# Performance work log

Hardware: AMD Instinct MI355X
Metric: run time of the kernel (lower is better)

Reference implementation:

```python
import jax, jax.numpy as jnp
import numpy as np

NUM_TOPICS = 100
VOCAB = 8192
MC_N = 20
MD_N = 20
LAMBDA_D = 0.7
LAMBDA_A = 100.0
WARMUP_RATIO = 0.5
NUM_EPOCHS = 200


def setup_inputs() -> dict:
    key = jax.random.key(0)
    k1, k2 = jax.random.split(key)
    beta = jax.random.normal(k1, (NUM_TOPICS, VOCAB), dtype=jnp.float32)
    W = jax.random.uniform(k2, (VOCAB, VOCAB), dtype=jnp.float32)
    # fill_diagonal_(1) in __init__
    d = jnp.arange(VOCAB)
    W = W.at[d, d].set(1.0)
    return {"beta": beta, "coherence_weight": W, "epoch": 120}


def reference(beta, coherence_weight, epoch):
    K, V = beta.shape
    rows = jnp.arange(K)[:, None]

    # --- Mc: top-Mc_n mask -> additive -99999 on non-topk entries ---
    _, mc_idx = jax.lax.top_k(beta, MC_N)                      # [K, Mc_n]
    Mc = jnp.zeros_like(beta).at[rows, mc_idx].set(1.0)        # [K, V]
    Mc_add = (1.0 - Mc) * (-99999.0)

    # softmax over masked beta is detached in the original
    p = jax.lax.stop_gradient(jax.nn.softmax(beta + Mc_add, axis=1))
    M = p @ coherence_weight                                    # [K, V]

    # row-wise min-max normalize, then Wc = 1 - normalized
    m_min = jnp.min(M, axis=1, keepdims=True)
    m_max = jnp.max(M, axis=1, keepdims=True)
    Wc = 1.0 - (M - m_min) / (m_max - m_min)

    loss = 100.0 * jax.nn.softmax(beta, axis=1) ** 2 * Wc       # [K, V]

    # --- diversity mask Md (lambda_d > 0.5 branch) ---
    _, md_idx = jax.lax.top_k(beta, MD_N)
    Md_mask = jnp.zeros_like(beta).at[rows, md_idx].set(1.0)    # [K, V]
    # Md[t, v] = any other row has v in its top-Md_n
    col_sum = jnp.sum(Md_mask, axis=0)                          # [V]
    Md = (col_sum[None, :] - Md_mask) > 0                       # [K, V] bool

    pos = jnp.sum(jnp.where(Md, loss, 0.0))
    neg = jnp.sum(jnp.where(Md, 0.0, loss))
    total = (pos * LAMBDA_D + neg * (1.0 - LAMBDA_D)) * 2.0

    warmup_epochs = int(WARMUP_RATIO * NUM_EPOCHS)              # 100
    lambda_a_delta = LAMBDA_A / warmup_epochs
    lambda_a = epoch * lambda_a_delta if epoch < warmup_epochs else LAMBDA_A
    return lambda_a * total
```

## Files before the change

kernel.cpp:

```cpp
#include <hip/hip_runtime.h>
#include <math.h>

#define NT 100
#define VOCAB 8192
#define TOPN 20
#define CHUNKS 8
#define CCOLS (VOCAB / CHUNKS)
#define CAP 4096

__global__ __launch_bounds__(256) void topk_kernel(
    const float* __restrict__ beta,
    int*   __restrict__ top_idx,
    float* __restrict__ top_p,
    float* __restrict__ rowstats)
{
    const int k = blockIdx.x;
    const int t = threadIdx.x;

    __shared__ float sred[4];
    __shared__ int   sredi[4];
    __shared__ float s_T;
    __shared__ int   s_base;
    __shared__ float cu[CAP];
    __shared__ unsigned short ci[CAP];
    __shared__ float s_winv[TOPN];
    __shared__ int   s_wini[TOPN];
    __shared__ float s_ps;

    const float* row = beta + (size_t)k * VOCAB;

    float4 r[8];
    float mx = -INFINITY;
#pragma unroll
    for (int i = 0; i < 8; ++i) {
        r[i] = *reinterpret_cast<const float4*>(row + (size_t)(i * 256 + t) * 4);
        mx = fmaxf(mx, fmaxf(fmaxf(r[i].x, r[i].y), fmaxf(r[i].z, r[i].w)));
    }
#pragma unroll
    for (int off = 32; off >= 1; off >>= 1) mx = fmaxf(mx, __shfl_down(mx, off));
    if ((t & 63) == 0) sred[t >> 6] = mx;
    __syncthreads();
    const float rowmax = fmaxf(fmaxf(sred[0], sred[1]), fmaxf(sred[2], sred[3]));

    float T = rowmax - 2.0f;
    for (int guard = 0; guard < 64; ++guard) {
        int c = 0;
#pragma unroll
        for (int i = 0; i < 8; ++i) {
            c += (r[i].x >= T) ? 1 : 0;
            c += (r[i].y >= T) ? 1 : 0;
            c += (r[i].z >= T) ? 1 : 0;
            c += (r[i].w >= T) ? 1 : 0;
        }
#pragma unroll
        for (int off = 32; off >= 1; off >>= 1) c += __shfl_down(c, off);
        if ((t & 63) == 0) sredi[t >> 6] = c;
        __syncthreads();
        const int cnt = sredi[0] + sredi[1] + sredi[2] + sredi[3];
        if (cnt >= TOPN) { if (t == 0) s_T = T; break; }
        T -= 0.5f;
        __syncthreads();
    }
    if (t == 0) s_base = 0;
    __syncthreads();
    T = s_T;

#pragma unroll
    for (int i = 0; i < 8; ++i) {
#pragma unroll
        for (int e = 0; e < 4; ++e) {
            const float v = (&r[i].x)[e];
            const int idx = (i * 256 + t) * 4 + e;
            const bool pr = (v >= T);
            const unsigned long long mask = __ballot(pr);
            const int lane = t & 63;
            const int pre = __popcll(mask & ((1ull << lane) - 1ull));
            int base = 0;
            if (lane == 0) base = atomicAdd(&s_base, __popcll(mask));
            base = __shfl(base, 0);
            if (pr) {
                const int p = base + pre;
                if (p < CAP) { cu[p] = v; ci[p] = (unsigned short)idx; }
            }
        }
    }
    __syncthreads();
    const int ncand = min(s_base, CAP);

    if (t < 64) {
        for (int it = 0; it < TOPN; ++it) {
            float bv = -INFINITY; int bp = -1;
            for (int p = t; p < ncand; p += 64) {
                const float v = cu[p];
                if (v > bv) { bv = v; bp = p; }
            }
#pragma unroll
            for (int off = 32; off >= 1; off >>= 1) {
                const float ov = __shfl_down(bv, off);
                const int   op = __shfl_down(bp, off);
                if (ov > bv) { bv = ov; bp = op; }
            }
            bp = __shfl(bp, 0);
            bv = __shfl(bv, 0);
            if (t == 0) { s_winv[it] = bv; s_wini[it] = ci[bp]; }
            cu[bp] = -INFINITY;
        }
    }
    __syncthreads();

    if (t == 0) {
        float ps = 0.f;
#pragma unroll
        for (int j = 0; j < TOPN; ++j) ps += expf(s_winv[j] - rowmax);
        s_ps = ps;
    }
    __syncthreads();
    if (t < TOPN) {
        top_idx[k * TOPN + t] = s_wini[t];
        top_p[k * TOPN + t]   = expf(s_winv[t] - rowmax) / s_ps;
    }

    float se = 0.f;
#pragma unroll
    for (int i = 0; i < 8; ++i) {
        se += expf(r[i].x - rowmax);
        se += expf(r[i].y - rowmax);
        se += expf(r[i].z - rowmax);
        se += expf(r[i].w - rowmax);
    }
#pragma unroll
    for (int off = 32; off >= 1; off >>= 1) se += __shfl_down(se, off);
    if ((t & 63) == 0) sred[t >> 6] = se;
    __syncthreads();
    if (t == 0) {
        rowstats[2 * k + 0] = rowmax;
        rowstats[2 * k + 1] = sred[0] + sred[1] + sred[2] + sred[3];
    }
}

__global__ __launch_bounds__(256) void fused_kernel(
    const float* __restrict__ beta,
    const float* __restrict__ W,
    const int*   __restrict__ top_idx,
    const float* __restrict__ top_p,
    const float* __restrict__ rowstats,
    float* __restrict__ mmpart,
    float* __restrict__ parts)
{
    const int b = blockIdx.x;
    const int k = b / CHUNKS;
    const int c = b % CHUNKS;
    const int t = threadIdx.x;

    __shared__ int   sIdx[TOPN];
    __shared__ float sP[TOPN];
    __shared__ int   cnt[CCOLS];
    __shared__ float sA[4], sB[4], sC[4], sD[4], sE[4], sF[4];

    if (t < TOPN) { sIdx[t] = top_idx[k * TOPN + t]; sP[t] = top_p[k * TOPN + t]; }
#pragma unroll
    for (int i = 0; i < CCOLS / 256; ++i) cnt[i * 256 + t] = 0;
    __syncthreads();

    const int lo = c * CCOLS;
    for (int e = t; e < NT * TOPN; e += 256) {
        const int v = top_idx[e] - lo;
        if ((unsigned)v < (unsigned)CCOLS) atomicAdd(&cnt[v], 1);
    }
    __syncthreads();
    if (t < TOPN) {
        const int v = sIdx[t] - lo;
        if ((unsigned)v < (unsigned)CCOLS) atomicSub(&cnt[v], 1);
    }

    int   idx_r[TOPN];
    float p_r[TOPN];
#pragma unroll
    for (int j = 0; j < TOPN; ++j) { idx_r[j] = sIdx[j]; p_r[j] = sP[j]; }

    const int col = lo + t * 4;
    float4 m = make_float4(0.f, 0.f, 0.f, 0.f);
#pragma unroll
    for (int j = 0; j < TOPN; ++j) {
        const float4 w = *reinterpret_cast<const float4*>(W + (size_t)idx_r[j] * VOCAB + col);
        const float pj = p_r[j];
        m.x += pj * w.x; m.y += pj * w.y; m.z += pj * w.z; m.w += pj * w.w;
    }

    float mn  = fminf(fminf(m.x, m.y), fminf(m.z, m.w));
    float mxv = fmaxf(fmaxf(m.x, m.y), fmaxf(m.z, m.w));

    const float rmax = rowstats[2 * k + 0];
    const float rinv = 1.0f / rowstats[2 * k + 1];
    const float4 bv = *reinterpret_cast<const float4*>(beta + (size_t)k * VOCAB + col);
    float4 w4;
    w4.x = expf(bv.x - rmax) * rinv;  w4.x = 100.f * w4.x * w4.x;
    w4.y = expf(bv.y - rmax) * rinv;  w4.y = 100.f * w4.y * w4.y;
    w4.z = expf(bv.z - rmax) * rinv;  w4.z = 100.f * w4.z * w4.z;
    w4.w = expf(bv.w - rmax) * rinv;  w4.w = 100.f * w4.w * w4.w;

    __syncthreads();

    float Apos = 0.f, Bpos = 0.f, Aneg = 0.f, Bneg = 0.f;
    {
        const int lc = t * 4;
        if (cnt[lc + 0] > 0) { Apos += w4.x; Bpos += w4.x * m.x; } else { Aneg += w4.x; Bneg += w4.x * m.x; }
        if (cnt[lc + 1] > 0) { Apos += w4.y; Bpos += w4.y * m.y; } else { Aneg += w4.y; Bneg += w4.y * m.y; }
        if (cnt[lc + 2] > 0) { Apos += w4.z; Bpos += w4.z * m.z; } else { Aneg += w4.z; Bneg += w4.z * m.z; }
        if (cnt[lc + 3] > 0) { Apos += w4.w; Bpos += w4.w * m.w; } else { Aneg += w4.w; Bneg += w4.w * m.w; }
    }

#pragma unroll
    for (int off = 32; off >= 1; off >>= 1) {
        mn   = fminf(mn,  __shfl_down(mn,  off));
        mxv  = fmaxf(mxv, __shfl_down(mxv, off));
        Apos += __shfl_down(Apos, off);
        Bpos += __shfl_down(Bpos, off);
        Aneg += __shfl_down(Aneg, off);
        Bneg += __shfl_down(Bneg, off);
    }
    if ((t & 63) == 0) {
        const int w = t >> 6;
        sA[w] = mn; sB[w] = mxv; sC[w] = Apos; sD[w] = Bpos; sE[w] = Aneg; sF[w] = Bneg;
    }
    __syncthreads();
    if (t == 0) {
        const int o = (k * CHUNKS + c);
        mmpart[o * 2 + 0] = fminf(fminf(sA[0], sA[1]), fminf(sA[2], sA[3]));
        mmpart[o * 2 + 1] = fmaxf(fmaxf(sB[0], sB[1]), fmaxf(sB[2], sB[3]));
        parts[o * 4 + 0] = sC[0] + sC[1] + sC[2] + sC[3];
        parts[o * 4 + 1] = sD[0] + sD[1] + sD[2] + sD[3];
        parts[o * 4 + 2] = sE[0] + sE[1] + sE[2] + sE[3];
        parts[o * 4 + 3] = sF[0] + sF[1] + sF[2] + sF[3];
    }
}

__global__ __launch_bounds__(128) void finalize_kernel(
    const float* __restrict__ mmpart,
    const float* __restrict__ parts,
    const int*   __restrict__ epoch,
    float* __restrict__ out)
{
    const int t = threadIdx.x;
    __shared__ float sp[128], sn[128];
    float pos = 0.f, neg = 0.f;
    if (t < NT) {
        const int k = t;
        float mn = INFINITY, mxv = -INFINITY;
        float Apos = 0.f, Bpos = 0.f, Aneg = 0.f, Bneg = 0.f;
        for (int c = 0; c < CHUNKS; ++c) {
            const int o = k * CHUNKS + c;
            mn  = fminf(mn,  mmpart[o * 2 + 0]);
            mxv = fmaxf(mxv, mmpart[o * 2 + 1]);
            Apos += parts[o * 4 + 0];
            Bpos += parts[o * 4 + 1];
            Aneg += parts[o * 4 + 2];
            Bneg += parts[o * 4 + 3];
        }
        const float inv = 1.0f / (mxv - mn);
        pos = Apos - inv * (Bpos - mn * Apos);
        neg = Aneg - inv * (Bneg - mn * Aneg);
    }
    sp[t] = pos; sn[t] = neg;
    __syncthreads();
    if (t == 0) {
        float P = 0.f, N = 0.f;
        for (int i = 0; i < NT; ++i) { P += sp[i]; N += sn[i]; }
        const float total = (P * 0.7f + N * 0.3f) * 2.0f;
        const int e = *epoch;
        const float la = (e < 100) ? (float)e : 100.0f;
        *out = la * total;
    }
}

extern "C" void kernel_launch(void* const* d_in, const int* in_sizes, int n_in,
                              void* d_out, int out_size, void* d_ws, size_t ws_size,
                              hipStream_t stream)
{
    (void)in_sizes; (void)n_in; (void)out_size; (void)ws_size;
    const float* beta  = (const float*)d_in[0];
    const float* W     = (const float*)d_in[1];
    const int*   epoch = (const int*)d_in[2];
    float* out = (float*)d_out;

    char* ws = (char*)d_ws;
    int*   top_idx  = (int*)ws;    ws += NT * TOPN * sizeof(int);
    float* top_p    = (float*)ws;  ws += NT * TOPN * sizeof(float);
    float* rowstats = (float*)ws;  ws += NT * 2 * sizeof(float);
    float* mmpart   = (float*)ws;  ws += NT * CHUNKS * 2 * sizeof(float);
    float* parts    = (float*)ws;  ws += NT * CHUNKS * 4 * sizeof(float);

    topk_kernel<<<NT, 256, 0, stream>>>(beta, top_idx, top_p, rowstats);
    fused_kernel<<<NT * CHUNKS, 256, 0, stream>>>(beta, W, top_idx, top_p, rowstats, mmpart, parts);
    finalize_kernel<<<1, 128, 0, stream>>>(mmpart, parts, epoch, out);
}
```

Before: 53.67 us.

## Fuse topk, coherence and finalize into one cooperative kernel with grid syncs

Replaces the three-kernel pipeline with a single cooperative kernel of 400 blocks. Each block computes a chunk-local top-20 and local softmax stats, then a grid sync lets one block per row merge the candidates. Column counts go into a global atomic histogram, and a last grid sync hands the final reduction to block 0. This removes launch gaps and the per-block histogram rebuild, at the cost of grid-wide barriers and a serial 20-iteration top-k per block. If the cooperative launch fails, it falls back to a two-kernel path that finalizes through a last-block ticket counter.

Result: slower. 177.6 us (+231.0%).

```diff
diff --git a/kernel.cpp b/kernel.cpp
--- a/kernel.cpp
+++ b/kernel.cpp
@@ -1,21 +1,281 @@
 #include <hip/hip_runtime.h>
+#include <hip/hip_cooperative_groups.h>
 #include <math.h>
+
+namespace cg = cooperative_groups;
 
 #define NT 100
 #define VOCAB 8192
 #define TOPN 20
-#define CHUNKS 8
-#define CCOLS (VOCAB / CHUNKS)
+
+#define CHUNKS 4
+#define CCOLS 2048
+#define NB (NT * CHUNKS)
+
+#define FB_CHUNKS 8
+#define FB_CCOLS 1024
+#define FB_NB (NT * FB_CHUNKS)
 #define CAP 4096
 
-__global__ __launch_bounds__(256) void topk_kernel(
+__global__ __launch_bounds__(256) void coherence_all(
+    const float* __restrict__ beta,
+    const float* __restrict__ W,
+    const int*   __restrict__ epoch,
+    float* __restrict__ out,
+    int*   __restrict__ col_cnt,
+    float* __restrict__ sl_val,
+    int*   __restrict__ sl_idx,
+    float* __restrict__ sl_max,
+    float* __restrict__ sl_sum,
+    int*   __restrict__ top_idx,
+    float* __restrict__ top_p,
+    float* __restrict__ rowstats,
+    float* __restrict__ part6)
+{
+    cg::grid_group grid = cg::this_grid();
+    const int b = blockIdx.x;
+    const int t = threadIdx.x;
+    const int k = b / CHUNKS;
+    const int c = b % CHUNKS;
+
+    __shared__ float srow[CCOLS];
+    __shared__ float sredf[4];
+    __shared__ int   sredi[4];
+    __shared__ float s_winv[TOPN];
+    __shared__ int   s_wini[TOPN];
+    __shared__ float s_ps;
+    __shared__ float cval[CHUNKS * TOPN];
+    __shared__ int   cgidx[CHUNKS * TOPN];
+    __shared__ float sP[TOPN];
+    __shared__ int   sI[TOPN];
+    __shared__ float sA[4], sB[4], sC[4], sD[4], sE[4], sF[4];
+    __shared__ float spd[128], snd[128];
+
+    if (b < VOCAB / 256) col_cnt[b * 256 + t] = 0;
+
+    const int col0 = c * CCOLS;
+    const float* brow = beta + (size_t)k * VOCAB + col0;
+
+    float4 r0 = *reinterpret_cast<const float4*>(brow + t * 4);
+    float4 r1 = *reinterpret_cast<const float4*>(brow + (256 + t) * 4);
+    *reinterpret_cast<float4*>(srow + t * 4)         = r0;
+    *reinterpret_cast<float4*>(srow + (256 + t) * 4) = r1;
+
+    float mx = fmaxf(fmaxf(fmaxf(r0.x, r0.y), fmaxf(r0.z, r0.w)),
+                     fmaxf(fmaxf(r1.x, r1.y), fmaxf(r1.z, r1.w)));
+#pragma unroll
+    for (int off = 32; off >= 1; off >>= 1) mx = fmaxf(mx, __shfl_down(mx, off));
+    if ((t & 63) == 0) sredf[t >> 6] = mx;
+    __syncthreads();
+    const float smax = fmaxf(fmaxf(sredf[0], sredf[1]), fmaxf(sredf[2], sredf[3]));
+    __syncthreads();
+
+    float se = expf(r0.x - smax) + expf(r0.y - smax) + expf(r0.z - smax) + expf(r0.w - smax)
+             + expf(r1.x - smax) + expf(r1.y - smax) + expf(r1.z - smax) + expf(r1.w - smax);
+#pragma unroll
+    for (int off = 32; off >= 1; off >>= 1) se += __shfl_down(se, off);
+    if ((t & 63) == 0) sredf[t >> 6] = se;
+    __syncthreads();
+    const float ssum = sredf[0] + sredf[1] + sredf[2] + sredf[3];
+    __syncthreads();
+
+    for (int it = 0; it < TOPN; ++it) {
+        float bvv = -INFINITY; int bi = 0x7fffffff;
+#pragma unroll
+        for (int e = 0; e < CCOLS / 256; ++e) {
+            const int idx = e * 256 + t;
+            const float v = srow[idx];
+            if (v > bvv || (v == bvv && idx < bi)) { bvv = v; bi = idx; }
+        }
+#pragma unroll
+        for (int off = 32; off >= 1; off >>= 1) {
+            const float ov = __shfl_down(bvv, off);
+            const int   oi = __shfl_down(bi, off);
+            if (ov > bvv || (ov == bvv && oi < bi)) { bvv = ov; bi = oi; }
+        }
+        if ((t & 63) == 0) { sredf[t >> 6] = bvv; sredi[t >> 6] = bi; }
+        __syncthreads();
+        if (t == 0) {
+            float mv = sredf[0]; int mi = sredi[0];
+#pragma unroll
+            for (int w = 1; w < 4; ++w)
+                if (sredf[w] > mv || (sredf[w] == mv && sredi[w] < mi)) { mv = sredf[w]; mi = sredi[w]; }
+            s_winv[it] = mv;
+            s_wini[it] = col0 + mi;
+            srow[mi] = -INFINITY;
+        }
+        __syncthreads();
+    }
+    if (t < TOPN) {
+        sl_val[b * TOPN + t] = s_winv[t];
+        sl_idx[b * TOPN + t] = s_wini[t];
+    }
+    if (t == 0) { sl_max[b] = smax; sl_sum[b] = ssum; }
+
+    grid.sync();
+
+    if (b < NT) {
+        if (t < CHUNKS * TOPN) {
+            cval[t]  = sl_val[b * CHUNKS * TOPN + t];
+            cgidx[t] = sl_idx[b * CHUNKS * TOPN + t];
+        }
+        __syncthreads();
+        if (t < 64) {
+            for (int it = 0; it < TOPN; ++it) {
+                float bvv = -INFINITY; int bp = -1; int bgi = 0x7fffffff;
+                for (int p = t; p < CHUNKS * TOPN; p += 64) {
+                    const float v = cval[p];
+                    const int  gi = cgidx[p];
+                    if (v > bvv || (v == bvv && gi < bgi)) { bvv = v; bp = p; bgi = gi; }
+                }
+#pragma unroll
+                for (int off = 32; off >= 1; off >>= 1) {
+                    const float ov = __shfl_down(bvv, off);
+                    const int   op = __shfl_down(bp, off);
+                    const int   og = __shfl_down(bgi, off);
+                    if (ov > bvv || (ov == bvv && og < bgi)) { bvv = ov; bp = op; bgi = og; }
+                }
+                bp = __shfl(bp, 0);
+                if (t == 0) { s_winv[it] = bvv; s_wini[it] = bgi; }
+                cval[bp] = -INFINITY;
+            }
+        }
+        __syncthreads();
+        if (t == 0) {
+            const float rowmax = s_winv[0];
+            float denom = 0.f;
+#pragma unroll
+            for (int j = 0; j < TOPN; ++j) denom += expf(s_winv[j] - rowmax);
+            float rowsum = 0.f;
+            for (int s = 0; s < CHUNKS; ++s)
+                rowsum += sl_sum[b * CHUNKS + s] * expf(sl_max[b * CHUNKS + s] - rowmax);
+            rowstats[2 * b + 0] = rowmax;
+            rowstats[2 * b + 1] = rowsum;
+            s_ps = denom;
+        }
+        __syncthreads();
+        if (t < TOPN) {
+            const int gi = s_wini[t];
+            top_idx[b * TOPN + t] = gi;
+            top_p[b * TOPN + t]   = expf(s_winv[t] - s_winv[0]) / s_ps;
+            atomicAdd(&col_cnt[gi], 1);
+        }
+    }
+
+    grid.sync();
+
+    if (t < TOPN) { sI[t] = top_idx[k * TOPN + t]; sP[t] = top_p[k * TOPN + t]; }
+    __syncthreads();
+
+    int   idx_r[TOPN];
+    float p_r[TOPN];
+#pragma unroll
+    for (int j = 0; j < TOPN; ++j) { idx_r[j] = sI[j]; p_r[j] = sP[j]; }
+
+    const float rmax = rowstats[2 * k + 0];
+    const float rinv = 1.0f / rowstats[2 * k + 1];
+
+    float mn = INFINITY, mxv = -INFINITY;
+    float Apos = 0.f, Bpos = 0.f, Aneg = 0.f, Bneg = 0.f;
+
+#pragma unroll
+    for (int rep = 0; rep < 2; ++rep) {
+        const int col = col0 + (rep * 256 + t) * 4;
+        float4 m = make_float4(0.f, 0.f, 0.f, 0.f);
+#pragma unroll
+        for (int j = 0; j < TOPN; ++j) {
+            const float4 w = *reinterpret_cast<const float4*>(W + (size_t)idx_r[j] * VOCAB + col);
+            const float pj = p_r[j];
+            m.x += pj * w.x; m.y += pj * w.y; m.z += pj * w.z; m.w += pj * w.w;
+        }
+        mn  = fminf(mn,  fminf(fminf(m.x, m.y), fminf(m.z, m.w)));
+        mxv = fmaxf(mxv, fmaxf(fmaxf(m.x, m.y), fmaxf(m.z, m.w)));
+
+        const float4 bv = *reinterpret_cast<const float4*>(beta + (size_t)k * VOCAB + col);
+        float4 w4;
+        w4.x = expf(bv.x - rmax) * rinv;  w4.x = 100.f * w4.x * w4.x;
+        w4.y = expf(bv.y - rmax) * rinv;  w4.y = 100.f * w4.y * w4.y;
+        w4.z = expf(bv.z - rmax) * rinv;  w4.z = 100.f * w4.z * w4.z;
+        w4.w = expf(bv.w - rmax) * rinv;  w4.w = 100.f * w4.w * w4.w;
+
+        const int4 cnt4 = *reinterpret_cast<const int4*>(col_cnt + col);
+        int own0 = 0, own1 = 0, own2 = 0, own3 = 0;
+#pragma unroll
+        for (int j = 0; j < TOPN; ++j) {
+            own0 |= (idx_r[j] == col + 0) ? 1 : 0;
+            own1 |= (idx_r[j] == col + 1) ? 1 : 0;
+            own2 |= (idx_r[j] == col + 2) ? 1 : 0;
+            own3 |= (idx_r[j] == col + 3) ? 1 : 0;
+        }
+        if (cnt4.x - own0 > 0) { Apos += w4.x; Bpos += w4.x * m.x; } else { Aneg += w4.x; Bneg += w4.x * m.x; }
+        if (cnt4.y - own1 > 0) { Apos += w4.y; Bpos += w4.y * m.y; } else { Aneg += w4.y; Bneg += w4.y * m.y; }
+        if (cnt4.z - own2 > 0) { Apos += w4.z; Bpos += w4.z * m.z; } else { Aneg += w4.z; Bneg += w4.z * m.z; }
+        if (cnt4.w - own3 > 0) { Apos += w4.w; Bpos += w4.w * m.w; } else { Aneg += w4.w; Bneg += w4.w * m.w; }
+    }
+
+#pragma unroll
+    for (int off = 32; off >= 1; off >>= 1) {
+        mn   = fminf(mn,  __shfl_down(mn,  off));
+        mxv  = fmaxf(mxv, __shfl_down(mxv, off));
+        Apos += __shfl_down(Apos, off);
+        Bpos += __shfl_down(Bpos, off);
+        Aneg += __shfl_down(Aneg, off);
+        Bneg += __shfl_down(Bneg, off);
+    }
+    if ((t & 63) == 0) {
+        const int w = t >> 6;
+        sA[w] = mn; sB[w] = mxv; sC[w] = Apos; sD[w] = Bpos; sE[w] = Aneg; sF[w] = Bneg;
+    }
+    __syncthreads();
+    if (t == 0) {
+        part6[b * 6 + 0] = fminf(fminf(sA[0], sA[1]), fminf(sA[2], sA[3]));
+        part6[b * 6 + 1] = fmaxf(fmaxf(sB[0], sB[1]), fmaxf(sB[2], sB[3]));
+        part6[b * 6 + 2] = sC[0] + sC[1] + sC[2] + sC[3];
+        part6[b * 6 + 3] = sD[0] + sD[1] + sD[2] + sD[3];
+        part6[b * 6 + 4] = sE[0] + sE[1] + sE[2] + sE[3];
+        part6[b * 6 + 5] = sF[0] + sF[1] + sF[2] + sF[3];
+    }
+
+    grid.sync();
+
+    if (b == 0) {
+        float pos = 0.f, neg = 0.f;
+        if (t < NT) {
+            float mn2 = INFINITY, mx2 = -INFINITY;
+            float Ap = 0.f, Bp = 0.f, An = 0.f, Bn = 0.f;
+            for (int cc = 0; cc < CHUNKS; ++cc) {
+                const float* p6 = part6 + (size_t)(t * CHUNKS + cc) * 6;
+                mn2 = fminf(mn2, p6[0]);
+                mx2 = fmaxf(mx2, p6[1]);
+                Ap += p6[2]; Bp += p6[3]; An += p6[4]; Bn += p6[5];
+            }
+            const float inv = 1.0f / (mx2 - mn2);
+            pos = Ap - inv * (Bp - mn2 * Ap);
+            neg = An - inv * (Bn - mn2 * An);
+        }
+        if (t < 128) { spd[t] = pos; snd[t] = neg; }
+        __syncthreads();
+        if (t == 0) {
+            float P = 0.f, N = 0.f;
+            for (int i = 0; i < NT; ++i) { P += spd[i]; N += snd[i]; }
+            const float total = (P * 0.7f + N * 0.3f) * 2.0f;
+            const int e = *epoch;
+            const float la = (e < 100) ? (float)e : 100.0f;
+            *out = la * total;
+        }
+    }
+}
+
+__global__ __launch_bounds__(256) void fb_topk_kernel(
     const float* __restrict__ beta,
     int*   __restrict__ top_idx,
     float* __restrict__ top_p,
-    float* __restrict__ rowstats)
+    float* __restrict__ rowstats,
+    unsigned* __restrict__ counter)
 {
     const int k = blockIdx.x;
     const int t = threadIdx.x;
+    if (k == 0 && t == 0) *counter = 0;
 
     __shared__ float sred[4];
     __shared__ int   sredi[4];
@@ -138,39 +398,43 @@
     }
 }
 
-__global__ __launch_bounds__(256) void fused_kernel(
+__global__ __launch_bounds__(256) void fb_fused_kernel(
     const float* __restrict__ beta,
     const float* __restrict__ W,
     const int*   __restrict__ top_idx,
     const float* __restrict__ top_p,
     const float* __restrict__ rowstats,
-    float* __restrict__ mmpart,
-    float* __restrict__ parts)
+    const int*   __restrict__ epoch,
+    float* __restrict__ part6,
+    unsigned* __restrict__ counter,
+    float* __restrict__ out)
 {
     const int b = blockIdx.x;
-    const int k = b / CHUNKS;
-    const int c = b % CHUNKS;
+    const int k = b / FB_CHUNKS;
+    const int c = b % FB_CHUNKS;
     const int t = threadIdx.x;
 
     __shared__ int   sIdx[TOPN];
     __shared__ float sP[TOPN];
-    __shared__ int   cnt[CCOLS];
+    __shared__ int   cnt[FB_CCOLS];
     __shared__ float sA[4], sB[4], sC[4], sD[4], sE[4], sF[4];
+    __shared__ unsigned s_ticket;
+    __shared__ float spd[128], snd[128];
 
     if (t < TOPN) { sIdx[t] = top_idx[k * TOPN + t]; sP[t] = top_p[k * TOPN + t]; }
 #pragma unroll
-    for (int i = 0; i < CCOLS / 256; ++i) cnt[i * 256 + t] = 0;
-    __syncthreads();
-
-    const int lo = c * CCOLS;
+    for (int i = 0; i < FB_CCOLS / 256; ++i) cnt[i * 256 + t] = 0;
+    __syncthreads();
+
+    const int lo = c * FB_CCOLS;
     for (int e = t; e < NT * TOPN; e += 256) {
         const int v = top_idx[e] - lo;
-        if ((unsigned)v < (unsigned)CCOLS) atomicAdd(&cnt[v], 1);
+        if ((unsigned)v < (unsigned)FB_CCOLS) atomicAdd(&cnt[v], 1);
     }
     __syncthreads();
     if (t < TOPN) {
         const int v = sIdx[t] - lo;
-        if ((unsigned)v < (unsigned)CCOLS) atomicSub(&cnt[v], 1);
+        if ((unsigned)v < (unsigned)FB_CCOLS) atomicSub(&cnt[v], 1);
     }
 
     int   idx_r[TOPN];
@@ -225,51 +489,43 @@
     }
     __syncthreads();
     if (t == 0) {
-        const int o = (k * CHUNKS + c);
-        mmpart[o * 2 + 0] = fminf(fminf(sA[0], sA[1]), fminf(sA[2], sA[3]));
-        mmpart[o * 2 + 1] = fmaxf(fmaxf(sB[0], sB[1]), fmaxf(sB[2], sB[3]));
-        parts[o * 4 + 0] = sC[0] + sC[1] + sC[2] + sC[3];
-        parts[o * 4 + 1] = sD[0] + sD[1] + sD[2] + sD[3];
-        parts[o * 4 + 2] = sE[0] + sE[1] + sE[2] + sE[3];
-        parts[o * 4 + 3] = sF[0] + sF[1] + sF[2] + sF[3];
-    }
-}
-
-__global__ __launch_bounds__(128) void finalize_kernel(
-    const float* __restrict__ mmpart,
-    const float* __restrict__ parts,
-    const int*   __restrict__ epoch,
-    float* __restrict__ out)
-{
-    const int t = threadIdx.x;
-    __shared__ float sp[128], sn[128];
-    float pos = 0.f, neg = 0.f;
-    if (t < NT) {
-        const int k = t;
-        float mn = INFINITY, mxv = -INFINITY;
-        float Apos = 0.f, Bpos = 0.f, Aneg = 0.f, Bneg = 0.f;
-        for (int c = 0; c < CHUNKS; ++c) {
-            const int o = k * CHUNKS + c;
-            mn  = fminf(mn,  mmpart[o * 2 + 0]);
-            mxv = fmaxf(mxv, mmpart[o * 2 + 1]);
-            Apos += parts[o * 4 + 0];
-            Bpos += parts[o * 4 + 1];
-            Aneg += parts[o * 4 + 2];
-            Bneg += parts[o * 4 + 3];
-        }
-        const float inv = 1.0f / (mxv - mn);
-        pos = Apos - inv * (Bpos - mn * Apos);
-        neg = Aneg - inv * (Bneg - mn * Aneg);
-    }
-    sp[t] = pos; sn[t] = neg;
-    __syncthreads();
-    if (t == 0) {
-        float P = 0.f, N = 0.f;
-        for (int i = 0; i < NT; ++i) { P += sp[i]; N += sn[i]; }
-        const float total = (P * 0.7f + N * 0.3f) * 2.0f;
-        const int e = *epoch;
-        const float la = (e < 100) ? (float)e : 100.0f;
-        *out = la * total;
+        part6[b * 6 + 0] = fminf(fminf(sA[0], sA[1]), fminf(sA[2], sA[3]));
+        part6[b * 6 + 1] = fmaxf(fmaxf(sB[0], sB[1]), fmaxf(sB[2], sB[3]));
+        part6[b * 6 + 2] = sC[0] + sC[1] + sC[2] + sC[3];
+        part6[b * 6 + 3] = sD[0] + sD[1] + sD[2] + sD[3];
+        part6[b * 6 + 4] = sE[0] + sE[1] + sE[2] + sE[3];
+        part6[b * 6 + 5] = sF[0] + sF[1] + sF[2] + sF[3];
+    }
+
+    __threadfence();
+    if (t == 0) s_ticket = atomicAdd(counter, 1u);
+    __syncthreads();
+    if (s_ticket == FB_NB - 1) {
+        __threadfence();
+        float pos = 0.f, neg = 0.f;
+        if (t < NT) {
+            float mn2 = INFINITY, mx2 = -INFINITY;
+            float Ap = 0.f, Bp = 0.f, An = 0.f, Bn = 0.f;
+            for (int cc = 0; cc < FB_CHUNKS; ++cc) {
+                const float* p6 = part6 + (size_t)(t * FB_CHUNKS + cc) * 6;
+                mn2 = fminf(mn2, p6[0]);
+                mx2 = fmaxf(mx2, p6[1]);
+                Ap += p6[2]; Bp += p6[3]; An += p6[4]; Bn += p6[5];
+            }
+            const float inv = 1.0f / (mx2 - mn2);
+            pos = Ap - inv * (Bp - mn2 * Ap);
+            neg = An - inv * (Bn - mn2 * An);
+        }
+        if (t < 128) { spd[t] = pos; snd[t] = neg; }
+        __syncthreads();
+        if (t == 0) {
+            float P = 0.f, N = 0.f;
+            for (int i = 0; i < NT; ++i) { P += spd[i]; N += snd[i]; }
+            const float total = (P * 0.7f + N * 0.3f) * 2.0f;
+            const int e = *epoch;
+            const float la = (e < 100) ? (float)e : 100.0f;
+            *out = la * total;
+        }
     }
 }
 
@@ -284,13 +540,29 @@
     float* out = (float*)d_out;
 
     char* ws = (char*)d_ws;
+    int*   col_cnt  = (int*)ws;    ws += VOCAB * sizeof(int);
+    float* sl_val   = (float*)ws;  ws += NB * TOPN * sizeof(float);
+    int*   sl_idx   = (int*)ws;    ws += NB * TOPN * sizeof(int);
+    float* sl_max   = (float*)ws;  ws += NB * sizeof(float);
+    float* sl_sum   = (float*)ws;  ws += NB * sizeof(float);
     int*   top_idx  = (int*)ws;    ws += NT * TOPN * sizeof(int);
     float* top_p    = (float*)ws;  ws += NT * TOPN * sizeof(float);
     float* rowstats = (float*)ws;  ws += NT * 2 * sizeof(float);
-    float* mmpart   = (float*)ws;  ws += NT * CHUNKS * 2 * sizeof(float);
-    float* parts    = (float*)ws;  ws += NT * CHUNKS * 4 * sizeof(float);
-
-    topk_kernel<<<NT, 256, 0, stream>>>(beta, top_idx, top_p, rowstats);
-    fused_kernel<<<NT * CHUNKS, 256, 0, stream>>>(beta, W, top_idx, top_p, rowstats, mmpart, parts);
-    finalize_kernel<<<1, 128, 0, stream>>>(mmpart, parts, epoch, out);
+    float* part6    = (float*)ws;  ws += NB * 6 * sizeof(float);
+    float* fb_part6 = (float*)ws;  ws += FB_NB * 6 * sizeof(float);
+    unsigned* counter = (unsigned*)ws; ws += sizeof(unsigned);
+
+    void* args[] = {
+        (void*)&beta, (void*)&W, (void*)&epoch, (void*)&out,
+        (void*)&col_cnt, (void*)&sl_val, (void*)&sl_idx, (void*)&sl_max,
+        (void*)&sl_sum, (void*)&top_idx, (void*)&top_p, (void*)&rowstats,
+        (void*)&part6
+    };
+    hipError_t err = hipLaunchCooperativeKernel((const void*)coherence_all,
+                                                dim3(NB), dim3(256), args, 0, stream);
+    if (err != hipSuccess) {
+        fb_topk_kernel<<<NT, 256, 0, stream>>>(beta, top_idx, top_p, rowstats, counter);
+        fb_fused_kernel<<<FB_NB, 256, 0, stream>>>(beta, W, top_idx, top_p, rowstats,
+                                                   epoch, fb_part6, counter, out);
+    }
 }
```
